# Kernel tuning notes

Measured on AMD Instinct MI355X. Metric: run time of the kernel, lower is better.

Reference implementation:

```python
import jax, jax.numpy as jnp
import numpy as np

B = 2048        # batch
L = 64          # number of time points -> L-1 spline segments
IN = 32         # input_channels (== output_channels == evolver state_dim)
HID = 128       # hidden_channels
MID = 128       # hardcoded width of DynamicsTrajectoryDE.linear1
OUT = 32        # output_channels
EVOLVE = 5.0    # final time of the evolver ODE
ODE_STEPS = 10  # fixed RK4 steps for the evolver odeint


def setup_inputs() -> dict:
    key = jax.random.key(0)
    ks = jax.random.split(key, 13)
    s = 0.1  # matches nn.init.normal_(std=0.1) flavor; keeps tanh unsaturated
    return {
        "coeffs": jax.random.normal(ks[0], (B, L - 1, 4 * IN), jnp.float32) * 0.1,
        "W_init": jax.random.normal(ks[1], (IN, HID), jnp.float32) * s,
        "b_init": jnp.zeros((HID,), jnp.float32),
        "W1": jax.random.normal(ks[2], (HID, MID), jnp.float32) * s,
        "b1": jnp.zeros((MID,), jnp.float32),
        "W2": jax.random.normal(ks[3], (MID, IN * HID), jnp.float32) * s,
        "b2": jnp.zeros((IN * HID,), jnp.float32),
        "W_ro": jax.random.normal(ks[4], (HID, OUT), jnp.float32) * s,
        "b_ro": jnp.zeros((OUT,), jnp.float32),
        "We1": jax.random.normal(ks[5], (IN, HID), jnp.float32) * s,
        "be1": jnp.zeros((HID,), jnp.float32),
        "We2": jax.random.normal(ks[6], (HID, IN), jnp.float32) * s,
        "be2": jnp.zeros((IN,), jnp.float32),
    }


def reference(coeffs, W_init, b_init, W1, b1, W2, b2, W_ro, b_ro,
              We1, be1, We2, be2):
    Bn, n_seg, _ = coeffs.shape
    # cubic spline: per-segment X(t) = a + b*fr + c*fr^2 + d*fr^3 on unit grid
    a, b, c, d = jnp.split(coeffs, 4, axis=-1)  # each [B, n_seg, IN]

    def dX_dt(t):  # derivative of the spline at scalar time t
        seg = jnp.clip(jnp.floor(t).astype(jnp.int32), 0, n_seg - 1)
        fr = t - seg.astype(t.dtype)
        return b[:, seg] + 2.0 * c[:, seg] * fr + 3.0 * d[:, seg] * (fr * fr)

    # initial hidden state from X(interval[0]) = a of segment 0
    X0 = a[:, 0]                      # [B, IN]
    z0 = X0 @ W_init + b_init         # [B, HID]

    def cde_field(t, z):
        # DynamicsTrajectoryDE: linear -> relu -> linear -> tanh -> [B,HID,IN]
        g = jnp.tanh(jax.nn.relu(z @ W1 + b1) @ W2 + b2)
        g = g.reshape(Bn, HID, IN)
        return jnp.einsum('bhi,bi->bh', g, dX_dt(t))

    # cdeint over [0, L-1]: fixed-step RK4, dt = 1 per spline segment
    dt = jnp.float32(1.0)

    def rk4_step(z, t):
        k1 = cde_field(t, z)
        k2 = cde_field(t + dt * 0.5, z + dt * 0.5 * k1)
        k3 = cde_field(t + dt * 0.5, z + dt * 0.5 * k2)
        k4 = cde_field(t + dt, z + dt * k3)
        return z + (dt / 6.0) * (k1 + 2.0 * k2 + 2.0 * k3 + k4), None

    zT, _ = jax.lax.scan(rk4_step, z0, jnp.arange(n_seg, dtype=jnp.float32))
    pred_y = zT @ W_ro + b_ro         # [B, OUT]

    # odeint(evolver, pred_y, [0, evolve]) with autonomous 2-layer tanh MLP
    def ev(y):
        return jnp.tanh(y @ We1 + be1) @ We2 + be2

    h = jnp.float32(EVOLVE / ODE_STEPS)

    def ev_step(y, _):
        k1 = ev(y)
        k2 = ev(y + h * 0.5 * k1)
        k3 = ev(y + h * 0.5 * k2)
        k4 = ev(y + h * k3)
        return y + (h / 6.0) * (k1 + 2.0 * k2 + 2.0 * k3 + k4), None

    y, _ = jax.lax.scan(ev_step, pred_y, None, length=ODE_STEPS)
    return y
```

## Files before the change

### kernel.cpp

```cpp
#include <hip/hip_runtime.h>

#define NSEG 63

typedef float    f32x4  __attribute__((ext_vector_type(4)));
typedef _Float16 half8  __attribute__((ext_vector_type(8)));
typedef _Float16 half4v __attribute__((ext_vector_type(4)));

#define W2_ELEMS 524288
#define W1_ELEMS 16384
#define W1H_OFF (2*W2_ELEMS)
#define W1L_OFF (W1H_OFF + W1_ELEMS)
#define B2_OFF  (W1L_OFF + W1_ELEMS)

__device__ __forceinline__ float fast_tanh(float x){
  float e = __builtin_amdgcn_exp2f(x * 2.885390081777927f);
  float r = __builtin_amdgcn_rcpf(e + 1.0f);
  return fmaf(-2.0f, r, 1.0f);
}

__device__ __forceinline__ f32x4 sp4(float v){ f32x4 o = {v,v,v,v}; return o; }

__device__ __forceinline__ void dma16(const _Float16* g, _Float16* l){
  __builtin_amdgcn_global_load_lds(
      (const __attribute__((address_space(1))) unsigned int*)g,
      (__attribute__((address_space(3))) unsigned int*)l,
      16, 0, 0);
}

__global__ __launch_bounds__(256) void prep_kernel(const float* __restrict__ W1,
                                                   const float* __restrict__ W2,
                                                   const float* __restrict__ b2,
                                                   _Float16* __restrict__ ws){
  int idx = blockIdx.x*256 + threadIdx.x;
  if (idx < W2_ELEMS){
    int m = idx >> 12, col = idx & 4095;
    int h = col >> 5,  i = col & 31;
    int kt = m >> 5,   kk = m & 31;
    float w = W2[idx];
    _Float16 hi = (_Float16)w;
    int hg = h >> 4, n = h & 15;
    int kq = kk >> 3, kl = kk & 7;
    int pos = kt*131072 + i*4096 + hg*512
            + n*32 + (((kq + (n>>1)) & 3) << 3) + kl;
    ws[pos] = hi;
  } else if (idx < W2_ELEMS + W1_ELEMS){
    int j = idx - W2_ELEMS;
    int m = j >> 7, n = j & 127;
    float w = W1[j];
    _Float16 hi = (_Float16)w;
    _Float16 lo = (_Float16)(w - (float)hi);
    int pos = ((m>>5)*128 + n)*32 + (m&31);
    ws[W1H_OFF + pos] = hi;
    ws[W1L_OFF + pos] = lo;
  } else if (idx < W2_ELEMS + W1_ELEMS + 4096){
    int j = idx - (W2_ELEMS + W1_ELEMS);
    float* b2p = (float*)(ws + B2_OFF);
    b2p[(j & 31)*128 + (j >> 5)] = b2[j];
  }
}

__global__ __launch_bounds__(512) void cde_kernel(
    const float* __restrict__ coeffs,
    const float* __restrict__ W_init, const float* __restrict__ b_init,
    const float* __restrict__ b1,
    const float* __restrict__ W_ro,  const float* __restrict__ b_ro,
    const float* __restrict__ We1,   const float* __restrict__ be1,
    const float* __restrict__ We2,   const float* __restrict__ be2,
    const _Float16* __restrict__ wsw,
    float* __restrict__ out)
{
  __shared__ __align__(16) _Float16 W2L[3][8][4][512];
  __shared__ __align__(16) _Float16 Zs[16][136];
  __shared__ __align__(16) _Float16 Zl[16][136];
  __shared__ __align__(16) _Float16 Hs[16][136];
  __shared__ __align__(16) _Float16 Hl[16][136];
  __shared__ __align__(16) float dXT[3][32][16];
  __shared__ __align__(16) float zfb[16][128];
  __shared__ __align__(16) float ylds[16][32];
  __shared__ __align__(16) float b2L[4096];

  const int tid  = threadIdx.x;
  const int wave = tid >> 6;
  const int lane = tid & 63;
  const int q    = lane >> 4;
  const int ln16 = lane & 15;
  const int row4 = q * 4;
  const int bg   = blockIdx.x * 16;
  const int n0   = wave * 16;
  const int fo   = ln16*32 + (((q + (ln16>>1)) & 3) << 3);

  {
    const float* b2p = (const float*)(wsw + B2_OFF);
    #pragma unroll
    for (int j = 0; j < 8; ++j) b2L[tid + j*512] = b2p[tid + j*512];
  }
  {
    int r = tid >> 5, i = tid & 31;
    dXT[0][i][r] = coeffs[(size_t)(bg + r)*(NSEG*128) + i];
  }
  __syncthreads();

  {
    int r = tid >> 5, h0 = (tid & 31) * 4;
    f32x4 acc = *(const f32x4*)&b_init[h0];
    #pragma unroll 8
    for (int i = 0; i < 32; ++i)
      acc += sp4(dXT[0][i][r]) * (*(const f32x4*)&W_init[i*128 + h0]);
    *(f32x4*)&zfb[r][h0] = acc;
    half4v zh, zl;
    #pragma unroll
    for (int k = 0; k < 4; ++k){
      _Float16 hi = (_Float16)acc[k];
      zh[k] = hi; zl[k] = (_Float16)(acc[k] - (float)hi);
    }
    *(half4v*)&Zs[r][h0] = zh;
    *(half4v*)&Zl[r][h0] = zl;
  }

  half8 w1h[4], w1l[4];
  {
    const half8* W1h8 = (const half8*)(wsw + W1H_OFF);
    const half8* W1l8 = (const half8*)(wsw + W1L_OFF);
    #pragma unroll
    for (int kt = 0; kt < 4; ++kt){
      int fi = (kt*128 + n0 + ln16)*4 + q;
      w1h[kt] = W1h8[fi];
      w1l[kt] = W1l8[fi];
    }
  }
  const float b1v = b1[n0 + ln16];
  __syncthreads();

  f32x4 zb, za = sp4(0.0f);
  #pragma unroll
  for (int k = 0; k < 4; ++k)
    zb[k] = zfb[row4 + k][n0 + ln16];

  auto issue = [&](int i, int b){
    const _Float16* g = wsw + (i*128 + n0)*32 + lane*8;
    _Float16* l = &W2L[b][wave][0][0];
    #pragma unroll
    for (int kt = 0; kt < 4; ++kt)
      dma16(g + kt*131072, l + kt*512);
  };

  for (int t = 0; t < NSEG; ++t){
    {
      int r = tid >> 5, i = tid & 31;
      const float* base = coeffs + (size_t)(bg + r)*(NSEG*128) + (size_t)t*128;
      float bb = base[32+i], cc = base[64+i], dd = base[96+i];
      dXT[0][i][r] = bb;
      dXT[1][i][r] = bb + cc + 0.75f*dd;
      float d4;
      if (t < NSEG-1) d4 = base[128+32+i];
      else            d4 = bb + 2.0f*cc + 3.0f*dd;
      dXT[2][i][r] = d4;
    }

    #pragma unroll 1
    for (int s = 0; s < 4; ++s){
      issue(0, 0); issue(1, 1); issue(2, 2);

      {
        half8 a1h[4], a1l[4];
        #pragma unroll
        for (int kt = 0; kt < 4; ++kt){
          a1h[kt] = *(const half8*)&Zs[ln16][kt*32 + q*8];
          a1l[kt] = *(const half8*)&Zl[ln16][kt*32 + q*8];
        }
        f32x4 u0 = sp4(b1v), u1 = sp4(0.0f), u2 = sp4(0.0f);
        #pragma unroll
        for (int kt = 0; kt < 4; ++kt){
          u0 = __builtin_amdgcn_mfma_f32_16x16x32_f16(a1h[kt], w1h[kt], u0, 0, 0, 0);
          u1 = __builtin_amdgcn_mfma_f32_16x16x32_f16(a1l[kt], w1h[kt], u1, 0, 0, 0);
          u2 = __builtin_amdgcn_mfma_f32_16x16x32_f16(a1h[kt], w1l[kt], u2, 0, 0, 0);
        }
        #pragma unroll
        for (int r = 0; r < 4; ++r){
          float hv = u0[r] + u1[r] + u2[r];
          hv = hv > 0.0f ? hv : 0.0f;
          _Float16 hi = (_Float16)hv;
          Hs[row4 + r][n0 + ln16] = hi;
          Hl[row4 + r][n0 + ln16] = (_Float16)(hv - (float)hi);
        }
      }
      __syncthreads();

      half8 a2h[4], a2l[4];
      #pragma unroll
      for (int kt = 0; kt < 4; ++kt){
        a2h[kt] = *(const half8*)&Hs[ln16][kt*32 + q*8];
        a2l[kt] = *(const half8*)&Hl[ln16][kt*32 + q*8];
      }
      const int v = (s == 0) ? 0 : ((s == 3) ? 2 : 1);
      f32x4 dz = sp4(0.0f);

      auto body = [&](const _Float16* Wb, int i){
        float b2v = b2L[i*128 + n0 + ln16];
        half8 bf0 = *(const half8*)(Wb + fo);
        half8 bf1 = *(const half8*)(Wb +  512 + fo);
        half8 bf2 = *(const half8*)(Wb + 1024 + fo);
        half8 bf3 = *(const half8*)(Wb + 1536 + fo);
        f32x4 u0 = sp4(b2v), u1 = sp4(0.0f);
        u0 = __builtin_amdgcn_mfma_f32_16x16x32_f16(a2h[0], bf0, u0, 0, 0, 0);
        u1 = __builtin_amdgcn_mfma_f32_16x16x32_f16(a2l[0], bf0, u1, 0, 0, 0);
        u0 = __builtin_amdgcn_mfma_f32_16x16x32_f16(a2h[1], bf1, u0, 0, 0, 0);
        u1 = __builtin_amdgcn_mfma_f32_16x16x32_f16(a2l[1], bf1, u1, 0, 0, 0);
        u0 = __builtin_amdgcn_mfma_f32_16x16x32_f16(a2h[2], bf2, u0, 0, 0, 0);
        u1 = __builtin_amdgcn_mfma_f32_16x16x32_f16(a2l[2], bf2, u1, 0, 0, 0);
        u0 = __builtin_amdgcn_mfma_f32_16x16x32_f16(a2h[3], bf3, u0, 0, 0, 0);
        u1 = __builtin_amdgcn_mfma_f32_16x16x32_f16(a2l[3], bf3, u1, 0, 0, 0);
        f32x4 dxv = *(const f32x4*)&dXT[v][i][row4];
        #pragma unroll
        for (int r = 0; r < 4; ++r)
          dz[r] = fmaf(fast_tanh(u0[r] + u1[r]), dxv[r], dz[r]);
      };

      {
        int b = 0;
        #pragma unroll 1
        for (int i = 0; i < 30; ++i){
          asm volatile("s_waitcnt vmcnt(8)" ::: "memory");
          body(&W2L[b][wave][0][0], i);
          if (i <= 28) issue(i + 3, b);
          b = (b == 2) ? 0 : b + 1;
        }
        asm volatile("s_waitcnt vmcnt(4)" ::: "memory");
        body(&W2L[0][wave][0][0], 30);
        asm volatile("s_waitcnt vmcnt(0)" ::: "memory");
        body(&W2L[1][wave][0][0], 31);
      }

      const float wk = (s == 3) ? 1.0f : 2.0f;
      #pragma unroll
      for (int k = 0; k < 4; ++k){
        float zan = (s == 0) ? dz[k] : za[k] + wk*dz[k];
        za[k] = zan;
        float zs;
        if (s == 3){ zb[k] += zan*(1.0f/6.0f); zs = zb[k]; }
        else if (s == 2) zs = zb[k] + dz[k];
        else             zs = zb[k] + 0.5f*dz[k];
        _Float16 hi = (_Float16)zs;
        Zs[row4 + k][n0 + ln16] = hi;
        Zl[row4 + k][n0 + ln16] = (_Float16)(zs - (float)hi);
      }
      __syncthreads();
    }
  }

  #pragma unroll
  for (int k = 0; k < 4; ++k)
    zfb[row4 + k][n0 + ln16] = zb[k];
  __syncthreads();

  const int r = tid >> 5, c = tid & 31;
  float yb = 0.0f, yac = 0.0f;
  {
    float yv = b_ro[c];
    #pragma unroll 8
    for (int h = 0; h < 128; ++h)
      yv = fmaf(zfb[r][h], W_ro[h*32 + c], yv);
    ylds[r][c] = yv;
    yb = yv;
  }
  __syncthreads();

  for (int st = 0; st < 10; ++st){
    #pragma unroll 1
    for (int s = 0; s < 4; ++s){
      {
        int rr = tid >> 5, m0 = (tid & 31) * 4;
        f32x4 acc = *(const f32x4*)&be1[m0];
        #pragma unroll 4
        for (int i = 0; i < 32; ++i)
          acc += sp4(ylds[rr][i]) * (*(const f32x4*)&We1[i*128 + m0]);
        f32x4 tt;
        tt.x = fast_tanh(acc.x); tt.y = fast_tanh(acc.y);
        tt.z = fast_tanh(acc.z); tt.w = fast_tanh(acc.w);
        *(f32x4*)&b2L[rr*128 + m0] = tt;
      }
      __syncthreads();
      {
        float kv = be2[c];
        #pragma unroll 8
        for (int m = 0; m < 128; ++m)
          kv = fmaf(b2L[r*128 + m], We2[m*32 + c], kv);
        float ysn;
        if      (s == 0){ yac = kv;        ysn = yb + 0.25f*kv; }
        else if (s == 1){ yac += 2.0f*kv;  ysn = yb + 0.25f*kv; }
        else if (s == 2){ yac += 2.0f*kv;  ysn = yb + 0.5f*kv;  }
        else            { yac += kv;       yb += yac*(1.0f/12.0f); ysn = yb; }
        ylds[r][c] = ysn;
      }
      __syncthreads();
    }
  }
  out[(size_t)(bg + r)*32 + c] = yb;
}

extern "C" void kernel_launch(void* const* d_in, const int* in_sizes, int n_in,
                              void* d_out, int out_size, void* d_ws, size_t ws_size,
                              hipStream_t stream){
  const float* coeffs = (const float*)d_in[0];
  const float* W_init = (const float*)d_in[1];
  const float* b_init = (const float*)d_in[2];
  const float* W1     = (const float*)d_in[3];
  const float* b1     = (const float*)d_in[4];
  const float* W2     = (const float*)d_in[5];
  const float* b2     = (const float*)d_in[6];
  const float* W_ro   = (const float*)d_in[7];
  const float* b_ro   = (const float*)d_in[8];
  const float* We1    = (const float*)d_in[9];
  const float* be1    = (const float*)d_in[10];
  const float* We2    = (const float*)d_in[11];
  const float* be2    = (const float*)d_in[12];
  _Float16* ws        = (_Float16*)d_ws;

  prep_kernel<<<2128, 256, 0, stream>>>(W1, W2, b2, ws);
  cde_kernel<<<128, 512, 0, stream>>>(coeffs, W_init, b_init, b1, W_ro, b_ro,
                                      We1, be1, We2, be2, ws, (float*)d_out);
}
```

Before: 3.172 ms.

## Process 32 batch rows per block to reuse W2 tiles and drop hi/lo H split

Each block now handles 32 batch rows instead of 16, so every W2 tile streamed into LDS feeds two MFMA row groups. This halves both the W2 traffic per sample and the grid size, from 128 to 64 blocks. The low-precision correction term for the hidden activations H is also dropped, so the second GEMM runs a single fp16 MFMA per tile instead of a hi/lo pair. zfb and ylds now alias the W2 staging buffer to save LDS. Accuracy may drop from losing the H low part, and with only 64 blocks many CUs on the device sit idle.

```diff
diff --git a/kernel.cpp b/kernel.cpp
--- a/kernel.cpp
+++ b/kernel.cpp
@@ -70,13 +70,10 @@
     float* __restrict__ out)
 {
   __shared__ __align__(16) _Float16 W2L[3][8][4][512];
-  __shared__ __align__(16) _Float16 Zs[16][136];
-  __shared__ __align__(16) _Float16 Zl[16][136];
-  __shared__ __align__(16) _Float16 Hs[16][136];
-  __shared__ __align__(16) _Float16 Hl[16][136];
-  __shared__ __align__(16) float dXT[3][32][16];
-  __shared__ __align__(16) float zfb[16][128];
-  __shared__ __align__(16) float ylds[16][32];
+  __shared__ __align__(16) _Float16 Zs[32][136];
+  __shared__ __align__(16) _Float16 Zl[32][136];
+  __shared__ __align__(16) _Float16 Hs[32][136];
+  __shared__ __align__(16) float dXT[3][32][32];
   __shared__ __align__(16) float b2L[4096];
 
   const int tid  = threadIdx.x;
@@ -85,28 +82,35 @@
   const int q    = lane >> 4;
   const int ln16 = lane & 15;
   const int row4 = q * 4;
-  const int bg   = blockIdx.x * 16;
+  const int bg   = blockIdx.x * 32;
   const int n0   = wave * 16;
   const int fo   = ln16*32 + (((q + (ln16>>1)) & 3) << 3);
 
+  float* zfb  = (float*)&W2L[0][0][0][0];
+  float* ylds = zfb + 4096;
+
   {
     const float* b2p = (const float*)(wsw + B2_OFF);
     #pragma unroll
     for (int j = 0; j < 8; ++j) b2L[tid + j*512] = b2p[tid + j*512];
   }
-  {
-    int r = tid >> 5, i = tid & 31;
+  #pragma unroll
+  for (int j = 0; j < 2; ++j){
+    int idx = tid + j*512;
+    int r = idx >> 5, i = idx & 31;
     dXT[0][i][r] = coeffs[(size_t)(bg + r)*(NSEG*128) + i];
   }
   __syncthreads();
 
-  {
-    int r = tid >> 5, h0 = (tid & 31) * 4;
+  #pragma unroll
+  for (int j = 0; j < 2; ++j){
+    int idx = tid + j*512;
+    int r = idx >> 5, h0 = (idx & 31) * 4;
     f32x4 acc = *(const f32x4*)&b_init[h0];
     #pragma unroll 8
     for (int i = 0; i < 32; ++i)
       acc += sp4(dXT[0][i][r]) * (*(const f32x4*)&W_init[i*128 + h0]);
-    *(f32x4*)&zfb[r][h0] = acc;
+    *(f32x4*)&zfb[r*128 + h0] = acc;
     half4v zh, zl;
     #pragma unroll
     for (int k = 0; k < 4; ++k){
@@ -131,10 +135,13 @@
   const float b1v = b1[n0 + ln16];
   __syncthreads();
 
-  f32x4 zb, za = sp4(0.0f);
-  #pragma unroll
-  for (int k = 0; k < 4; ++k)
-    zb[k] = zfb[row4 + k][n0 + ln16];
+  f32x4 zbA, zbB, zaA = sp4(0.0f), zaB = sp4(0.0f);
+  #pragma unroll
+  for (int k = 0; k < 4; ++k){
+    zbA[k] = zfb[(row4 + k)*128 + n0 + ln16];
+    zbB[k] = zfb[(16 + row4 + k)*128 + n0 + ln16];
+  }
+  __syncthreads();
 
   auto issue = [&](int i, int b){
     const _Float16* g = wsw + (i*128 + n0)*32 + lane*8;
@@ -145,8 +152,10 @@
   };
 
   for (int t = 0; t < NSEG; ++t){
-    {
-      int r = tid >> 5, i = tid & 31;
+    #pragma unroll
+    for (int j = 0; j < 2; ++j){
+      int idx = tid + j*512;
+      int r = idx >> 5, i = idx & 31;
       const float* base = coeffs + (size_t)(bg + r)*(NSEG*128) + (size_t)t*128;
       float bb = base[32+i], cc = base[64+i], dd = base[96+i];
       dXT[0][i][r] = bb;
@@ -161,12 +170,12 @@
     for (int s = 0; s < 4; ++s){
       issue(0, 0); issue(1, 1); issue(2, 2);
 
-      {
+      auto gemm1 = [&](int ro){
         half8 a1h[4], a1l[4];
         #pragma unroll
         for (int kt = 0; kt < 4; ++kt){
-          a1h[kt] = *(const half8*)&Zs[ln16][kt*32 + q*8];
-          a1l[kt] = *(const half8*)&Zl[ln16][kt*32 + q*8];
+          a1h[kt] = *(const half8*)&Zs[ro + ln16][kt*32 + q*8];
+          a1l[kt] = *(const half8*)&Zl[ro + ln16][kt*32 + q*8];
         }
         f32x4 u0 = sp4(b1v), u1 = sp4(0.0f), u2 = sp4(0.0f);
         #pragma unroll
@@ -179,21 +188,21 @@
         for (int r = 0; r < 4; ++r){
           float hv = u0[r] + u1[r] + u2[r];
           hv = hv > 0.0f ? hv : 0.0f;
-          _Float16 hi = (_Float16)hv;
-          Hs[row4 + r][n0 + ln16] = hi;
-          Hl[row4 + r][n0 + ln16] = (_Float16)(hv - (float)hi);
-        }
-      }
+          Hs[ro + row4 + r][n0 + ln16] = (_Float16)hv;
+        }
+      };
+      gemm1(0);
+      gemm1(16);
       __syncthreads();
 
-      half8 a2h[4], a2l[4];
+      half8 a2hA[4], a2hB[4];
       #pragma unroll
       for (int kt = 0; kt < 4; ++kt){
-        a2h[kt] = *(const half8*)&Hs[ln16][kt*32 + q*8];
-        a2l[kt] = *(const half8*)&Hl[ln16][kt*32 + q*8];
+        a2hA[kt] = *(const half8*)&Hs[ln16][kt*32 + q*8];
+        a2hB[kt] = *(const half8*)&Hs[16 + ln16][kt*32 + q*8];
       }
       const int v = (s == 0) ? 0 : ((s == 3) ? 2 : 1);
-      f32x4 dz = sp4(0.0f);
+      f32x4 dzA = sp4(0.0f), dzB = sp4(0.0f);
 
       auto body = [&](const _Float16* Wb, int i){
         float b2v = b2L[i*128 + n0 + ln16];
@@ -201,19 +210,22 @@
         half8 bf1 = *(const half8*)(Wb +  512 + fo);
         half8 bf2 = *(const half8*)(Wb + 1024 + fo);
         half8 bf3 = *(const half8*)(Wb + 1536 + fo);
-        f32x4 u0 = sp4(b2v), u1 = sp4(0.0f);
-        u0 = __builtin_amdgcn_mfma_f32_16x16x32_f16(a2h[0], bf0, u0, 0, 0, 0);
-        u1 = __builtin_amdgcn_mfma_f32_16x16x32_f16(a2l[0], bf0, u1, 0, 0, 0);
-        u0 = __builtin_amdgcn_mfma_f32_16x16x32_f16(a2h[1], bf1, u0, 0, 0, 0);
-        u1 = __builtin_amdgcn_mfma_f32_16x16x32_f16(a2l[1], bf1, u1, 0, 0, 0);
-        u0 = __builtin_amdgcn_mfma_f32_16x16x32_f16(a2h[2], bf2, u0, 0, 0, 0);
-        u1 = __builtin_amdgcn_mfma_f32_16x16x32_f16(a2l[2], bf2, u1, 0, 0, 0);
-        u0 = __builtin_amdgcn_mfma_f32_16x16x32_f16(a2h[3], bf3, u0, 0, 0, 0);
-        u1 = __builtin_amdgcn_mfma_f32_16x16x32_f16(a2l[3], bf3, u1, 0, 0, 0);
-        f32x4 dxv = *(const f32x4*)&dXT[v][i][row4];
+        f32x4 uA = sp4(b2v), uB = sp4(b2v);
+        uA = __builtin_amdgcn_mfma_f32_16x16x32_f16(a2hA[0], bf0, uA, 0, 0, 0);
+        uB = __builtin_amdgcn_mfma_f32_16x16x32_f16(a2hB[0], bf0, uB, 0, 0, 0);
+        uA = __builtin_amdgcn_mfma_f32_16x16x32_f16(a2hA[1], bf1, uA, 0, 0, 0);
+        uB = __builtin_amdgcn_mfma_f32_16x16x32_f16(a2hB[1], bf1, uB, 0, 0, 0);
+        uA = __builtin_amdgcn_mfma_f32_16x16x32_f16(a2hA[2], bf2, uA, 0, 0, 0);
+        uB = __builtin_amdgcn_mfma_f32_16x16x32_f16(a2hB[2], bf2, uB, 0, 0, 0);
+        uA = __builtin_amdgcn_mfma_f32_16x16x32_f16(a2hA[3], bf3, uA, 0, 0, 0);
+        uB = __builtin_amdgcn_mfma_f32_16x16x32_f16(a2hB[3], bf3, uB, 0, 0, 0);
+        f32x4 dxvA = *(const f32x4*)&dXT[v][i][row4];
+        f32x4 dxvB = *(const f32x4*)&dXT[v][i][16 + row4];
         #pragma unroll
-        for (int r = 0; r < 4; ++r)
-          dz[r] = fmaf(fast_tanh(u0[r] + u1[r]), dxv[r], dz[r]);
+        for (int r = 0; r < 4; ++r){
+          dzA[r] = fmaf(fast_tanh(uA[r]), dxvA[r], dzA[r]);
+          dzB[r] = fmaf(fast_tanh(uB[r]), dxvB[r], dzB[r]);
+        }
       };
 
       {
@@ -234,68 +246,91 @@
       const float wk = (s == 3) ? 1.0f : 2.0f;
       #pragma unroll
       for (int k = 0; k < 4; ++k){
-        float zan = (s == 0) ? dz[k] : za[k] + wk*dz[k];
-        za[k] = zan;
-        float zs;
-        if (s == 3){ zb[k] += zan*(1.0f/6.0f); zs = zb[k]; }
-        else if (s == 2) zs = zb[k] + dz[k];
-        else             zs = zb[k] + 0.5f*dz[k];
-        _Float16 hi = (_Float16)zs;
-        Zs[row4 + k][n0 + ln16] = hi;
-        Zl[row4 + k][n0 + ln16] = (_Float16)(zs - (float)hi);
+        float zanA = (s == 0) ? dzA[k] : zaA[k] + wk*dzA[k];
+        zaA[k] = zanA;
+        float zsA;
+        if (s == 3){ zbA[k] += zanA*(1.0f/6.0f); zsA = zbA[k]; }
+        else if (s == 2) zsA = zbA[k] + dzA[k];
+        else             zsA = zbA[k] + 0.5f*dzA[k];
+        _Float16 hiA = (_Float16)zsA;
+        Zs[row4 + k][n0 + ln16] = hiA;
+        Zl[row4 + k][n0 + ln16] = (_Float16)(zsA - (float)hiA);
+        float zanB = (s == 0) ? dzB[k] : zaB[k] + wk*dzB[k];
+        zaB[k] = zanB;
+        float zsB;
+        if (s == 3){ zbB[k] += zanB*(1.0f/6.0f); zsB = zbB[k]; }
+        else if (s == 2) zsB = zbB[k] + dzB[k];
+        else             zsB = zbB[k] + 0.5f*dzB[k];
+        _Float16 hiB = (_Float16)zsB;
+        Zs[16 + row4 + k][n0 + ln16] = hiB;
+        Zl[16 + row4 + k][n0 + ln16] = (_Float16)(zsB - (float)hiB);
       }
       __syncthreads();
     }
   }
 
   #pragma unroll
-  for (int k = 0; k < 4; ++k)
-    zfb[row4 + k][n0 + ln16] = zb[k];
-  __syncthreads();
-
-  const int r = tid >> 5, c = tid & 31;
-  float yb = 0.0f, yac = 0.0f;
-  {
+  for (int k = 0; k < 4; ++k){
+    zfb[(row4 + k)*128 + n0 + ln16]      = zbA[k];
+    zfb[(16 + row4 + k)*128 + n0 + ln16] = zbB[k];
+  }
+  __syncthreads();
+
+  float yb[2], yac[2] = {0.0f, 0.0f};
+  #pragma unroll
+  for (int j = 0; j < 2; ++j){
+    int idx = tid + j*512;
+    int r = idx >> 5, c = idx & 31;
     float yv = b_ro[c];
     #pragma unroll 8
     for (int h = 0; h < 128; ++h)
-      yv = fmaf(zfb[r][h], W_ro[h*32 + c], yv);
-    ylds[r][c] = yv;
-    yb = yv;
+      yv = fmaf(zfb[r*128 + h], W_ro[h*32 + c], yv);
+    ylds[r*32 + c] = yv;
+    yb[j] = yv;
   }
   __syncthreads();
 
   for (int st = 0; st < 10; ++st){
     #pragma unroll 1
     for (int s = 0; s < 4; ++s){
-      {
-        int rr = tid >> 5, m0 = (tid & 31) * 4;
+      #pragma unroll
+      for (int j = 0; j < 2; ++j){
+        int idx = tid + j*512;
+        int rr = idx >> 5, m0 = (idx & 31) * 4;
         f32x4 acc = *(const f32x4*)&be1[m0];
         #pragma unroll 4
         for (int i = 0; i < 32; ++i)
-          acc += sp4(ylds[rr][i]) * (*(const f32x4*)&We1[i*128 + m0]);
+          acc += sp4(ylds[rr*32 + i]) * (*(const f32x4*)&We1[i*128 + m0]);
         f32x4 tt;
         tt.x = fast_tanh(acc.x); tt.y = fast_tanh(acc.y);
         tt.z = fast_tanh(acc.z); tt.w = fast_tanh(acc.w);
         *(f32x4*)&b2L[rr*128 + m0] = tt;
       }
       __syncthreads();
-      {
+      #pragma unroll
+      for (int j = 0; j < 2; ++j){
+        int idx = tid + j*512;
+        int r = idx >> 5, c = idx & 31;
         float kv = be2[c];
         #pragma unroll 8
         for (int m = 0; m < 128; ++m)
           kv = fmaf(b2L[r*128 + m], We2[m*32 + c], kv);
         float ysn;
-        if      (s == 0){ yac = kv;        ysn = yb + 0.25f*kv; }
-        else if (s == 1){ yac += 2.0f*kv;  ysn = yb + 0.25f*kv; }
-        else if (s == 2){ yac += 2.0f*kv;  ysn = yb + 0.5f*kv;  }
-        else            { yac += kv;       yb += yac*(1.0f/12.0f); ysn = yb; }
-        ylds[r][c] = ysn;
+        if      (s == 0){ yac[j] = kv;        ysn = yb[j] + 0.25f*kv; }
+        else if (s == 1){ yac[j] += 2.0f*kv;  ysn = yb[j] + 0.25f*kv; }
+        else if (s == 2){ yac[j] += 2.0f*kv;  ysn = yb[j] + 0.5f*kv;  }
+        else            { yac[j] += kv;       yb[j] += yac[j]*(1.0f/12.0f); ysn = yb[j]; }
+        ylds[r*32 + c] = ysn;
       }
       __syncthreads();
     }
   }
-  out[(size_t)(bg + r)*32 + c] = yb;
+  #pragma unroll
+  for (int j = 0; j < 2; ++j){
+    int idx = tid + j*512;
+    int r = idx >> 5, c = idx & 31;
+    out[(size_t)(bg + r)*32 + c] = yb[j];
+  }
 }
 
 extern "C" void kernel_launch(void* const* d_in, const int* in_sizes, int n_in,
@@ -317,6 +352,6 @@
   _Float16* ws        = (_Float16*)d_ws;
 
   prep_kernel<<<2128, 256, 0, stream>>>(W1, W2, b2, ws);
-  cde_kernel<<<128, 512, 0, stream>>>(coeffs, W_init, b_init, b1, W_ro, b_ro,
-                                      We1, be1, We2, be2, ws, (float*)d_out);
-}
+  cde_kernel<<<64, 512, 0, stream>>>(coeffs, W_init, b_init, b1, W_ro, b_ro,
+                                     We1, be1, We2, be2, ws, (float*)d_out);
+}
```

Measured after the change: 4.268 ms. +34.6%, slower.
